# Kernel tuning notes

Hardware: AMD Instinct MI355X
Metric: run time of the kernel (lower is better)

The kernel has to match this reference:

```python
import jax, jax.numpy as jnp
import numpy as np

N = 16384      # total nodes
SEQ = 512      # nodes per graph
NG = 32        # graphs (N = NG*SEQ)
D = 128        # dim_h
H = 8          # heads
E = 262144     # edges
BN_EPS = 1e-5


def _bn(x, g, b):
    # BatchNorm1d, training-mode stats over the node axis (biased var, as torch)
    mu = x.mean(axis=0)
    var = x.var(axis=0)
    return (x - mu) * jax.lax.rsqrt(var + BN_EPS) * g + b


def setup_inputs() -> dict:
    key = jax.random.key(0)
    ks = jax.random.split(key, 24)
    w = lambda k, shp: (jax.random.normal(k, shp, jnp.float32) * 0.05)
    x = jax.random.normal(ks[0], (N, D), jnp.float32)
    # within-graph edges: dst in same graph as src
    src = jax.random.randint(ks[1], (E,), 0, N, dtype=jnp.int32)
    dst = (src // SEQ) * SEQ + jax.random.randint(ks[2], (E,), 0, SEQ, dtype=jnp.int32)
    edge_index = jnp.stack([src, dst])
    edge_attr = jax.random.normal(ks[3], (E, D), jnp.float32)
    return {
        'x': x, 'edge_index': edge_index, 'edge_attr': edge_attr,
        'gin_w1': w(ks[4], (D, D)), 'gin_b1': jnp.zeros((D,), jnp.float32),
        'gin_w2': w(ks[5], (D, D)), 'gin_b2': jnp.zeros((D,), jnp.float32),
        'bn1l_g': jnp.ones((D,), jnp.float32), 'bn1l_b': jnp.zeros((D,), jnp.float32),
        'in_proj_w': w(ks[6], (3 * D, D)), 'in_proj_b': jnp.zeros((3 * D,), jnp.float32),
        'out_proj_w': w(ks[7], (D, D)), 'out_proj_b': jnp.zeros((D,), jnp.float32),
        'bn1a_g': jnp.ones((D,), jnp.float32), 'bn1a_b': jnp.zeros((D,), jnp.float32),
        'ff_w1': w(ks[8], (D, 2 * D)), 'ff_b1': jnp.zeros((2 * D,), jnp.float32),
        'ff_w2': w(ks[9], (2 * D, D)), 'ff_b2': jnp.zeros((D,), jnp.float32),
        'bn2_g': jnp.ones((D,), jnp.float32), 'bn2_b': jnp.zeros((D,), jnp.float32),
    }


def reference(x, edge_index, edge_attr, gin_w1, gin_b1, gin_w2, gin_b2,
              bn1l_g, bn1l_b, in_proj_w, in_proj_b, out_proj_w, out_proj_b,
              bn1a_g, bn1a_b, ff_w1, ff_b1, ff_w2, ff_b2, bn2_g, bn2_b):
    h_in1 = x
    src, dst = edge_index[0], edge_index[1]
    # --- local GINE: aggr_i = sum_{j->i} relu(x_j + e_ji); nn((1+eps)*x + aggr), eps=0
    msg = jax.nn.relu(x[src] + edge_attr)                 # [E, D]
    aggr = jax.ops.segment_sum(msg, dst, num_segments=N)  # [N, D]
    z = x + aggr
    h_local = jax.nn.relu(z @ gin_w1 + gin_b1) @ gin_w2 + gin_b2
    h_local = h_in1 + h_local                # residual (dropout=0)
    h_local = _bn(h_local, bn1l_g, bn1l_b)
    # --- global Transformer attention over dense batch (equal-size graphs => reshape)
    hd = x.reshape(NG, SEQ, D)
    qkv = hd @ in_proj_w.T + in_proj_b       # [NG, SEQ, 3D]
    q, k, v = jnp.split(qkv, 3, axis=-1)
    dh = D // H
    q = q.reshape(NG, SEQ, H, dh)
    k = k.reshape(NG, SEQ, H, dh)
    v = v.reshape(NG, SEQ, H, dh)
    scores = jnp.einsum('bqhd,bkhd->bhqk', q, k) / jnp.sqrt(jnp.float32(dh))
    attn = jax.nn.softmax(scores, axis=-1)
    o = jnp.einsum('bhqk,bkhd->bqhd', attn, v).reshape(NG, SEQ, D)
    h_attn = (o @ out_proj_w.T + out_proj_b).reshape(N, D)
    h_attn = h_in1 + h_attn                  # residual (attn_dropout=0)
    h_attn = _bn(h_attn, bn1a_g, bn1a_b)
    # --- combine + FFN block
    h = h_local + h_attn
    ff = jax.nn.relu(h @ ff_w1 + ff_b1) @ ff_w2 + ff_b2
    h = h + ff
    h = _bn(h, bn2_g, bn2_b)
    return h
```

## Files before the change

kernel.cpp:

```cpp
#include <hip/hip_runtime.h>


#define N_NODES 16384
#define SEQL    512
#define NGRAPH  32
#define DIM     128
#define NHEAD   8
#define DHEAD   16
#define NEDGE   262144
#define BUCKET  64

typedef __bf16 bf16;
typedef __bf16 bf16x8 __attribute__((ext_vector_type(8)));
typedef __bf16 bf16x4 __attribute__((ext_vector_type(4)));
typedef __bf16 bf16x2 __attribute__((ext_vector_type(2)));
typedef float  f32x4  __attribute__((ext_vector_type(4)));

__device__ inline f32x4 mfma16(bf16x8 a, bf16x8 b, f32x4 c) {
  return __builtin_amdgcn_mfma_f32_16x16x32_bf16(a, b, c, 0, 0, 0);
}

__device__ inline void stage_w(const bf16* __restrict__ src0, int stride, int tid,
                               bf16 (*Wlds)[136]) {
  int n = tid >> 1, ch = (tid & 1) * 64;
  const bf16* src = src0 + (size_t)n * stride + ch;
  bf16* dst = &Wlds[n][ch];
#pragma unroll
  for (int j = 0; j < 8; ++j)
    *(bf16x8*)(dst + j * 8) = *(const bf16x8*)(src + j * 8);
}

__global__ __launch_bounds__(256) void prep_k(
    const float* __restrict__ gw1, const float* __restrict__ gw2,
    const float* __restrict__ ipw, const float* __restrict__ opw,
    const float* __restrict__ fw1, const float* __restrict__ fw2,
    bf16* __restrict__ W, int* __restrict__ cnt, float* __restrict__ stats)
{
  int i = blockIdx.x * 256 + threadIdx.x;
  if (i < 16384) {
    W[(i & 127) * 128 + (i >> 7)] = (bf16)gw1[i];
  } else if (i < 32768) {
    int j = i - 16384;
    W[16384 + (j & 127) * 128 + (j >> 7)] = (bf16)gw2[j];
  } else if (i < 81920) {
    W[i] = (bf16)ipw[i - 32768];
  } else if (i < 98304) {
    W[i] = (bf16)opw[i - 81920];
  } else if (i < 131072) {
    int j = i - 98304;
    W[98304 + (j & 255) * 128 + (j >> 8)] = (bf16)fw1[j];
  } else if (i < 163840) {
    int j = i - 131072;
    W[131072 + (j & 127) * 256 + (j >> 7)] = (bf16)fw2[j];
  } else if (i < 163840 + 16384) {
    cnt[i - 163840] = 0;
  } else if (i < 163840 + 16384 + 768) {
    stats[i - 163840 - 16384] = 0.f;
  }
}

__global__ __launch_bounds__(256) void scatter_k(const int* __restrict__ ei,
                                                 int* __restrict__ cnt,
                                                 int2* __restrict__ se)
{
  int e = blockIdx.x * 256 + threadIdx.x;
  if (e < NEDGE) {
    int s = ei[e];
    int d = ei[NEDGE + e];
    int p = atomicAdd(&cnt[d], 1);
    if (p < BUCKET) se[(d << 6) + p] = make_int2(s, e);
  }
}

__global__ __launch_bounds__(256) void aggr_k(
    const float* __restrict__ x, const float* __restrict__ ea,
    const int* __restrict__ cnt, const int2* __restrict__ se,
    bf16* __restrict__ z)
{
  int node = blockIdx.x * 4 + (threadIdx.x >> 6);
  int lane = threadIdx.x & 63;
  int c = lane * 2;
  int n = cnt[node];
  if (n > BUCKET) n = BUCKET;
  int o0 = node << 6, o1 = o0 + n;
  float a0 = 0.f, a1 = 0.f;
  int j = o0;
  for (; j + 4 <= o1; j += 4) {
    int2 p0 = se[j], p1 = se[j + 1], p2 = se[j + 2], p3 = se[j + 3];
    float2 x0 = *(const float2*)(x + (size_t)p0.x * 128 + c);
    float2 e0 = *(const float2*)(ea + (size_t)p0.y * 128 + c);
    float2 x1 = *(const float2*)(x + (size_t)p1.x * 128 + c);
    float2 e1 = *(const float2*)(ea + (size_t)p1.y * 128 + c);
    float2 x2 = *(const float2*)(x + (size_t)p2.x * 128 + c);
    float2 e2 = *(const float2*)(ea + (size_t)p2.y * 128 + c);
    float2 x3 = *(const float2*)(x + (size_t)p3.x * 128 + c);
    float2 e3 = *(const float2*)(ea + (size_t)p3.y * 128 + c);
    a0 += fmaxf(x0.x + e0.x, 0.f) + fmaxf(x1.x + e1.x, 0.f) +
          fmaxf(x2.x + e2.x, 0.f) + fmaxf(x3.x + e3.x, 0.f);
    a1 += fmaxf(x0.y + e0.y, 0.f) + fmaxf(x1.y + e1.y, 0.f) +
          fmaxf(x2.y + e2.y, 0.f) + fmaxf(x3.y + e3.y, 0.f);
  }
  for (; j < o1; ++j) {
    int2 p = se[j];
    float2 xe = *(const float2*)(x + (size_t)p.x * 128 + c);
    float2 ae = *(const float2*)(ea + (size_t)p.y * 128 + c);
    a0 += fmaxf(xe.x + ae.x, 0.f);
    a1 += fmaxf(xe.y + ae.y, 0.f);
  }
  float2 xn = *(const float2*)(x + (size_t)node * 128 + c);
  *(bf16x2*)(z + (size_t)node * 128 + c) =
      (bf16x2){(bf16)(xn.x + a0), (bf16)(xn.y + a1)};
}

__global__ __launch_bounds__(256) void proj_k(
    const bf16* __restrict__ z, const float* __restrict__ x,
    const bf16* __restrict__ W,
    const float* __restrict__ gb1, const float* __restrict__ gb2,
    const float* __restrict__ ipb,
    float* __restrict__ hl, bf16* __restrict__ qb, bf16* __restrict__ kb,
    bf16* __restrict__ vb, float* __restrict__ stats)
{
  __shared__ bf16 Alds[32][136];
  __shared__ bf16 Wlds[128][136];
  __shared__ bf16 Tlds[32][136];
  __shared__ float slds[256];
  int tid = threadIdx.x;
  int wave = tid >> 6, lane = tid & 63, quad = lane >> 4, l16 = lane & 15;
  int rg = wave >> 1, chalf = wave & 1;
  int bid = blockIdx.x;

  if (bid < 512) {
    int m0 = bid * 32;
    slds[tid] = 0.f;
    {
      int r = tid >> 3, c16 = (tid & 7) * 16;
      const bf16* src = z + (size_t)(m0 + r) * 128 + c16;
      *(bf16x8*)&Alds[r][c16]     = *(const bf16x8*)src;
      *(bf16x8*)&Alds[r][c16 + 8] = *(const bf16x8*)(src + 8);
    }
    stage_w(W, 128, tid, Wlds);
    __syncthreads();
    f32x4 acc[4];
#pragma unroll
    for (int t = 0; t < 4; ++t) acc[t] = (f32x4){0.f, 0.f, 0.f, 0.f};
#pragma unroll
    for (int kt = 0; kt < 4; ++kt) {
      bf16x8 af = *(const bf16x8*)&Alds[rg * 16 + l16][kt * 32 + quad * 8];
#pragma unroll
      for (int nt = 0; nt < 4; ++nt) {
        bf16x8 bfr = *(const bf16x8*)&Wlds[chalf * 64 + nt * 16 + l16][kt * 32 + quad * 8];
        acc[nt] = mfma16(af, bfr, acc[nt]);
      }
    }
    __syncthreads();
    int rowl = rg * 16 + quad * 4;
#pragma unroll
    for (int nt = 0; nt < 4; ++nt) {
      int n = chalf * 64 + nt * 16 + l16;
      float bv = gb1[n];
#pragma unroll
      for (int r = 0; r < 4; ++r)
        Tlds[rowl + r][n] = (bf16)fmaxf(acc[nt][r] + bv, 0.f);
    }
    stage_w(W + 16384, 128, tid, Wlds);
    __syncthreads();
#pragma unroll
    for (int t = 0; t < 4; ++t) acc[t] = (f32x4){0.f, 0.f, 0.f, 0.f};
#pragma unroll
    for (int kt = 0; kt < 4; ++kt) {
      bf16x8 af = *(const bf16x8*)&Tlds[rg * 16 + l16][kt * 32 + quad * 8];
#pragma unroll
      for (int nt = 0; nt < 4; ++nt) {
        bf16x8 bfr = *(const bf16x8*)&Wlds[chalf * 64 + nt * 16 + l16][kt * 32 + quad * 8];
        acc[nt] = mfma16(af, bfr, acc[nt]);
      }
    }
    int rowb = m0 + rowl;
#pragma unroll
    for (int nt = 0; nt < 4; ++nt) {
      int n = chalf * 64 + nt * 16 + l16;
      float bv = gb2[n];
      float vals[4];
#pragma unroll
      for (int r = 0; r < 4; ++r) {
        float v = acc[nt][r] + bv + x[(size_t)(rowb + r) * 128 + n];
        vals[r] = v;
        hl[(size_t)(rowb + r) * 128 + n] = v;
      }
      float s = vals[0] + vals[1] + vals[2] + vals[3];
      float q2 = vals[0] * vals[0] + vals[1] * vals[1] +
                 vals[2] * vals[2] + vals[3] * vals[3];
      s += __shfl_xor(s, 16);  s += __shfl_xor(s, 32);
      q2 += __shfl_xor(q2, 16); q2 += __shfl_xor(q2, 32);
      if (quad == 0) {
        atomicAdd(&slds[n * 2], s);
        atomicAdd(&slds[n * 2 + 1], q2);
      }
    }
    __syncthreads();
    if (tid < 128) {
      atomicAdd(&stats[tid], slds[tid * 2]);
      atomicAdd(&stats[128 + tid], slds[tid * 2 + 1]);
    }
  } else {
    int m0 = (bid - 512) * 32;
    {
      int r = tid >> 3, c16 = (tid & 7) * 16;
      const float* src = x + (size_t)(m0 + r) * 128 + c16;
      float4 v0 = *(const float4*)(src);
      float4 v1 = *(const float4*)(src + 4);
      float4 v2 = *(const float4*)(src + 8);
      float4 v3 = *(const float4*)(src + 12);
      *(bf16x8*)&Alds[r][c16] =
          (bf16x8){(bf16)v0.x, (bf16)v0.y, (bf16)v0.z, (bf16)v0.w,
                   (bf16)v1.x, (bf16)v1.y, (bf16)v1.z, (bf16)v1.w};
      *(bf16x8*)&Alds[r][c16 + 8] =
          (bf16x8){(bf16)v2.x, (bf16)v2.y, (bf16)v2.z, (bf16)v2.w,
                   (bf16)v3.x, (bf16)v3.y, (bf16)v3.z, (bf16)v3.w};
    }
    for (int nc = 0; nc < 3; ++nc) {
      if (nc) __syncthreads();
      stage_w(W + 32768 + nc * 16384, 128, tid, Wlds);
      __syncthreads();
      f32x4 acc[4];
#pragma unroll
      for (int t = 0; t < 4; ++t) acc[t] = (f32x4){0.f, 0.f, 0.f, 0.f};
#pragma unroll
      for (int kt = 0; kt < 4; ++kt) {
        bf16x8 af = *(const bf16x8*)&Alds[rg * 16 + l16][kt * 32 + quad * 8];
#pragma unroll
        for (int nt = 0; nt < 4; ++nt) {
          bf16x8 bfr = *(const bf16x8*)&Wlds[chalf * 64 + nt * 16 + l16][kt * 32 + quad * 8];
          acc[nt] = mfma16(af, bfr, acc[nt]);
        }
      }
      bf16* obuf = (nc == 0) ? qb : ((nc == 1) ? kb : vb);
      int rowb = m0 + rg * 16 + quad * 4;
#pragma unroll
      for (int nt = 0; nt < 4; ++nt) {
        int n = chalf * 64 + nt * 16 + l16;
        float bv = ipb[nc * 128 + n];
#pragma unroll
        for (int r = 0; r < 4; ++r)
          obuf[(size_t)(rowb + r) * 128 + n] = (bf16)(acc[nt][r] + bv);
      }
    }
  }
}

template <int NCH, int KCH, bool RELU, int RESID, bool STATS, int OUTMODE>
__global__ __launch_bounds__(256) void gemm_k(
    const float* __restrict__ Aptr, const bf16* __restrict__ Wt,
    const float* __restrict__ bias, const float* __restrict__ resid,
    float* __restrict__ outF, bf16* __restrict__ oq, bf16* __restrict__ okk,
    bf16* __restrict__ ov, float* __restrict__ stats)
{
  constexpr int KIN = KCH * 128;
  constexpr int NLD = NCH * 128;
  __shared__ bf16 Alds[32][136];
  __shared__ bf16 Wlds[128][136];
  __shared__ float slds[256];
  int tid = threadIdx.x;
  int wave = tid >> 6, lane = tid & 63, quad = lane >> 4, l16 = lane & 15;
  int rg = wave >> 1, chalf = wave & 1;
  int m0 = blockIdx.x * 32;
  if (STATS) slds[tid] = 0.f;

  for (int nc = 0; nc < NCH; ++nc) {
    f32x4 acc[4];
#pragma unroll
    for (int t = 0; t < 4; ++t) acc[t] = (f32x4){0.f, 0.f, 0.f, 0.f};
    for (int kc = 0; kc < KCH; ++kc) {
      if (!(nc == 0 && kc == 0)) __syncthreads();
      if (nc == 0 || KCH > 1) {
        int r = tid >> 3, c16 = (tid & 7) * 16;
        const float* src = Aptr + (size_t)(m0 + r) * KIN + kc * 128 + c16;
        float4 v0 = *(const float4*)(src);
        float4 v1 = *(const float4*)(src + 4);
        float4 v2 = *(const float4*)(src + 8);
        float4 v3 = *(const float4*)(src + 12);
        *(bf16x8*)&Alds[r][c16] =
            (bf16x8){(bf16)v0.x, (bf16)v0.y, (bf16)v0.z, (bf16)v0.w,
                     (bf16)v1.x, (bf16)v1.y, (bf16)v1.z, (bf16)v1.w};
        *(bf16x8*)&Alds[r][c16 + 8] =
            (bf16x8){(bf16)v2.x, (bf16)v2.y, (bf16)v2.z, (bf16)v2.w,
                     (bf16)v3.x, (bf16)v3.y, (bf16)v3.z, (bf16)v3.w};
      }
      stage_w(Wt + (size_t)(nc * 128) * KIN + kc * 128, KIN, tid, Wlds);
      __syncthreads();
#pragma unroll
      for (int kt = 0; kt < 4; ++kt) {
        bf16x8 af = *(const bf16x8*)&Alds[rg * 16 + l16][kt * 32 + quad * 8];
#pragma unroll
        for (int nt = 0; nt < 4; ++nt) {
          bf16x8 bfr =
              *(const bf16x8*)&Wlds[chalf * 64 + nt * 16 + l16][kt * 32 + quad * 8];
          acc[nt] = mfma16(af, bfr, acc[nt]);
        }
      }
    }
    int rowb = m0 + rg * 16 + quad * 4;
#pragma unroll
    for (int nt = 0; nt < 4; ++nt) {
      int n = chalf * 64 + nt * 16 + l16;
      int gcol = nc * 128 + n;
      float bv = bias[gcol];
      float vals[4];
#pragma unroll
      for (int r = 0; r < 4; ++r) {
        float v = acc[nt][r] + bv;
        if (RELU) v = fmaxf(v, 0.f);
        if (RESID) v += resid[(size_t)(rowb + r) * 128 + n];
        vals[r] = v;
        if (OUTMODE == 0) {
          outF[(size_t)(rowb + r) * NLD + gcol] = v;
        } else {
          bf16* ob = (nc == 0) ? oq : ((nc == 1) ? okk : ov);
          ob[(size_t)(rowb + r) * 128 + n] = (bf16)v;
        }
      }
      if (STATS) {
        float s = vals[0] + vals[1] + vals[2] + vals[3];
        float q2 = vals[0] * vals[0] + vals[1] * vals[1] +
                   vals[2] * vals[2] + vals[3] * vals[3];
        s += __shfl_xor(s, 16);  s += __shfl_xor(s, 32);
        q2 += __shfl_xor(q2, 16); q2 += __shfl_xor(q2, 32);
        if (quad == 0) {
          atomicAdd(&slds[n * 2], s);
          atomicAdd(&slds[n * 2 + 1], q2);
        }
      }
    }
  }
  if (STATS) {
    __syncthreads();
    if (tid < 128) {
      atomicAdd(&stats[tid], slds[tid * 2]);
      atomicAdd(&stats[128 + tid], slds[tid * 2 + 1]);
    }
  }
}

__global__ __launch_bounds__(256) void attn_k(
    const bf16* __restrict__ qg, const bf16* __restrict__ kg,
    const bf16* __restrict__ vg, float* __restrict__ og)
{
  __shared__ bf16 Klds[512][24];
  __shared__ bf16 Vlds[16][520];
  __shared__ bf16 Plds[4][16][136];
  int b = blockIdx.x;
  int half = b & 1, hh = (b >> 1) & 7, g = b >> 4;
  int tid = threadIdx.x;
  const size_t gbase = (size_t)g * 512 * 128 + hh * 16;
  for (int r = tid; r < 512; r += 256) {
    const bf16* src = kg + gbase + (size_t)r * 128;
    *(bf16x8*)&Klds[r][0] = *(const bf16x8*)src;
    *(bf16x8*)&Klds[r][8] = *(const bf16x8*)(src + 8);
  }
  for (int r = tid; r < 512; r += 256) {
    const bf16* src = vg + gbase + (size_t)r * 128;
    bf16x8 v0 = *(const bf16x8*)src;
    bf16x8 v1 = *(const bf16x8*)(src + 8);
#pragma unroll
    for (int d = 0; d < 8; ++d) { Vlds[d][r] = v0[d]; Vlds[d + 8][r] = v1[d]; }
  }
  __syncthreads();
  int wave = tid >> 6, lane = tid & 63, quad = lane >> 4, l16 = lane & 15;
  const bf16x8 z8 = {};
  for (int it = 0; it < 4; ++it) {
    int qt = half * 16 + it * 4 + wave;
    bf16x8 qf = z8;
    if (quad < 2)
      qf = *(const bf16x8*)(qg + gbase + (size_t)(qt * 16 + l16) * 128 + quad * 8);
    f32x4 S[32];
#pragma unroll
    for (int jt = 0; jt < 32; ++jt) {
      bf16x8 kf = z8;
      if (quad < 2) kf = *(const bf16x8*)&Klds[jt * 16 + l16][quad * 8];
      S[jt] = mfma16(kf, qf, (f32x4){0.f, 0.f, 0.f, 0.f});
    }
    float s0 = 0.f, s1 = 0.f, s2 = 0.f, s3 = 0.f;
#pragma unroll
    for (int jt = 0; jt < 32; ++jt) {
      float e0 = __expf(S[jt][0] * 0.25f);
      float e1 = __expf(S[jt][1] * 0.25f);
      float e2 = __expf(S[jt][2] * 0.25f);
      float e3 = __expf(S[jt][3] * 0.25f);
      S[jt][0] = e0; S[jt][1] = e1; S[jt][2] = e2; S[jt][3] = e3;
      s0 += e0; s1 += e1; s2 += e2; s3 += e3;
    }
    float sm = (s0 + s1) + (s2 + s3);
    sm += __shfl_xor(sm, 16);
    sm += __shfl_xor(sm, 32);
    float rinv = 1.f / sm;
    f32x4 O = (f32x4){0.f, 0.f, 0.f, 0.f};
#pragma unroll
    for (int qd = 0; qd < 4; ++qd) {
#pragma unroll
      for (int jt2 = 0; jt2 < 8; ++jt2) {
        f32x4 sv = S[qd * 8 + jt2];
        bf16x4 pk = {(bf16)sv[0], (bf16)sv[1], (bf16)sv[2], (bf16)sv[3]};
        *(bf16x4*)&Plds[wave][l16][jt2 * 16 + quad * 4] = pk;
      }
#pragma unroll
      for (int kt = 0; kt < 4; ++kt) {
        bf16x8 pf = *(const bf16x8*)&Plds[wave][l16][kt * 32 + quad * 8];
        bf16x8 vf = *(const bf16x8*)&Vlds[l16][qd * 128 + kt * 32 + quad * 8];
        O = mfma16(vf, pf, O);
      }
    }
    *(float4*)(og + (size_t)(g * 512 + qt * 16 + l16) * 128 + hh * 16 + quad * 4) =
        make_float4(O[0] * rinv, O[1] * rinv, O[2] * rinv, O[3] * rinv);
  }
}

__global__ __launch_bounds__(256) void ffn_k(
    const float* __restrict__ hl, const float* __restrict__ ha,
    const bf16* __restrict__ W1, const bf16* __restrict__ W2,
    const float* __restrict__ fb1, const float* __restrict__ fb2,
    const float* __restrict__ stats,
    const float* __restrict__ g1v, const float* __restrict__ b1v,
    const float* __restrict__ g2v, const float* __restrict__ b2v,
    float* __restrict__ h2o, float* __restrict__ so)
{
  __shared__ float Hlds[32][132];
  __shared__ bf16 Ablds[32][136];
  __shared__ bf16 Wlds[128][136];
  __shared__ bf16 Tlds[32][264];
  __shared__ float sc1[128], sh1[128], sc2[128], sh2[128];
  __shared__ float slds[256];
  int tid = threadIdx.x;
  int wave = tid >> 6, lane = tid & 63, quad = lane >> 4, l16 = lane & 15;
  int rg = wave >> 1, chalf = wave & 1;
  int m0 = blockIdx.x * 32;
  slds[tid] = 0.f;
  if (tid < 128) {
    const float inv = 1.f / 16384.f;
    float mu = stats[tid] * inv;
    float var = stats[128 + tid] * inv - mu * mu;
    float s = g1v[tid] * rsqrtf(var + 1e-5f);
    sc1[tid] = s; sh1[tid] = b1v[tid] - mu * s;
    mu = stats[256 + tid] * inv;
    var = stats[384 + tid] * inv - mu * mu;
    s = g2v[tid] * rsqrtf(var + 1e-5f);
    sc2[tid] = s; sh2[tid] = b2v[tid] - mu * s;
  }
  __syncthreads();
  {
    int r = tid >> 3, c0 = (tid & 7) * 16;
    const float* pl = hl + (size_t)(m0 + r) * 128 + c0;
    const float* pa = ha + (size_t)(m0 + r) * 128 + c0;
#pragma unroll
    for (int j = 0; j < 16; j += 8) {
      float4 a0 = *(const float4*)(pl + j);
      float4 a1 = *(const float4*)(pl + j + 4);
      float4 c0v = *(const float4*)(pa + j);
      float4 c1v = *(const float4*)(pa + j + 4);
      int c = c0 + j;
      float h0 = a0.x * sc1[c]     + sh1[c]     + c0v.x * sc2[c]     + sh2[c];
      float h1 = a0.y * sc1[c + 1] + sh1[c + 1] + c0v.y * sc2[c + 1] + sh2[c + 1];
      float h2 = a0.z * sc1[c + 2] + sh1[c + 2] + c0v.z * sc2[c + 2] + sh2[c + 2];
      float h3 = a0.w * sc1[c + 3] + sh1[c + 3] + c0v.w * sc2[c + 3] + sh2[c + 3];
      float h4 = a1.x * sc1[c + 4] + sh1[c + 4] + c1v.x * sc2[c + 4] + sh2[c + 4];
      float h5 = a1.y * sc1[c + 5] + sh1[c + 5] + c1v.y * sc2[c + 5] + sh2[c + 5];
      float h6 = a1.z * sc1[c + 6] + sh1[c + 6] + c1v.z * sc2[c + 6] + sh2[c + 6];
      float h7 = a1.w * sc1[c + 7] + sh1[c + 7] + c1v.w * sc2[c + 7] + sh2[c + 7];
      *(float4*)&Hlds[r][c]     = make_float4(h0, h1, h2, h3);
      *(float4*)&Hlds[r][c + 4] = make_float4(h4, h5, h6, h7);
      *(bf16x8*)&Ablds[r][c] = (bf16x8){(bf16)h0, (bf16)h1, (bf16)h2, (bf16)h3,
                                        (bf16)h4, (bf16)h5, (bf16)h6, (bf16)h7};
    }
  }
  stage_w(W1, 128, tid, Wlds);
  __syncthreads();
  int rowl = rg * 16 + quad * 4;
  f32x4 acc[4];
#pragma unroll
  for (int t = 0; t < 4; ++t) acc[t] = (f32x4){0.f, 0.f, 0.f, 0.f};
#pragma unroll
  for (int kt = 0; kt < 4; ++kt) {
    bf16x8 af = *(const bf16x8*)&Ablds[rg * 16 + l16][kt * 32 + quad * 8];
#pragma unroll
    for (int nt = 0; nt < 4; ++nt) {
      bf16x8 bfr = *(const bf16x8*)&Wlds[chalf * 64 + nt * 16 + l16][kt * 32 + quad * 8];
      acc[nt] = mfma16(af, bfr, acc[nt]);
    }
  }
  __syncthreads();
#pragma unroll
  for (int nt = 0; nt < 4; ++nt) {
    int n = chalf * 64 + nt * 16 + l16;
    float bv = fb1[n];
#pragma unroll
    for (int r = 0; r < 4; ++r)
      Tlds[rowl + r][n] = (bf16)fmaxf(acc[nt][r] + bv, 0.f);
  }
  stage_w(W1 + 128 * 128, 128, tid, Wlds);
  __syncthreads();
#pragma unroll
  for (int t = 0; t < 4; ++t) acc[t] = (f32x4){0.f, 0.f, 0.f, 0.f};
#pragma unroll
  for (int kt = 0; kt < 4; ++kt) {
    bf16x8 af = *(const bf16x8*)&Ablds[rg * 16 + l16][kt * 32 + quad * 8];
#pragma unroll
    for (int nt = 0; nt < 4; ++nt) {
      bf16x8 bfr = *(const bf16x8*)&Wlds[chalf * 64 + nt * 16 + l16][kt * 32 + quad * 8];
      acc[nt] = mfma16(af, bfr, acc[nt]);
    }
  }
  __syncthreads();
#pragma unroll
  for (int nt = 0; nt < 4; ++nt) {
    int n = chalf * 64 + nt * 16 + l16;
    float bv = fb1[128 + n];
#pragma unroll
    for (int r = 0; r < 4; ++r)
      Tlds[rowl + r][128 + n] = (bf16)fmaxf(acc[nt][r] + bv, 0.f);
  }
  stage_w(W2, 256, tid, Wlds);
  __syncthreads();
#pragma unroll
  for (int t = 0; t < 4; ++t) acc[t] = (f32x4){0.f, 0.f, 0.f, 0.f};
#pragma unroll
  for (int kt = 0; kt < 4; ++kt) {
    bf16x8 af = *(const bf16x8*)&Tlds[rg * 16 + l16][kt * 32 + quad * 8];
#pragma unroll
    for (int nt = 0; nt < 4; ++nt) {
      bf16x8 bfr = *(const bf16x8*)&Wlds[chalf * 64 + nt * 16 + l16][kt * 32 + quad * 8];
      acc[nt] = mfma16(af, bfr, acc[nt]);
    }
  }
  __syncthreads();
  stage_w(W2 + 128, 256, tid, Wlds);
  __syncthreads();
#pragma unroll
  for (int kt = 0; kt < 4; ++kt) {
    bf16x8 af = *(const bf16x8*)&Tlds[rg * 16 + l16][128 + kt * 32 + quad * 8];
#pragma unroll
    for (int nt = 0; nt < 4; ++nt) {
      bf16x8 bfr = *(const bf16x8*)&Wlds[chalf * 64 + nt * 16 + l16][kt * 32 + quad * 8];
      acc[nt] = mfma16(af, bfr, acc[nt]);
    }
  }
  int rowb = m0 + rowl;
#pragma unroll
  for (int nt = 0; nt < 4; ++nt) {
    int n = chalf * 64 + nt * 16 + l16;
    float bv = fb2[n];
    float vals[4];
#pragma unroll
    for (int r = 0; r < 4; ++r) {
      float v = acc[nt][r] + bv + Hlds[rowl + r][n];
      vals[r] = v;
      h2o[(size_t)(rowb + r) * 128 + n] = v;
    }
    float s = vals[0] + vals[1] + vals[2] + vals[3];
    float q2 = vals[0] * vals[0] + vals[1] * vals[1] +
               vals[2] * vals[2] + vals[3] * vals[3];
    s += __shfl_xor(s, 16);  s += __shfl_xor(s, 32);
    q2 += __shfl_xor(q2, 16); q2 += __shfl_xor(q2, 32);
    if (quad == 0) {
      atomicAdd(&slds[n * 2], s);
      atomicAdd(&slds[n * 2 + 1], q2);
    }
  }
  __syncthreads();
  if (tid < 128) {
    atomicAdd(&so[tid], slds[tid * 2]);
    atomicAdd(&so[128 + tid], slds[tid * 2 + 1]);
  }
}

__global__ __launch_bounds__(256) void apply_k(
    const float* __restrict__ h2, const float* __restrict__ stats,
    const float* __restrict__ g, const float* __restrict__ b,
    float* __restrict__ out)
{
  __shared__ float sc[128], sh[128];
  int tid = threadIdx.x;
  if (tid < 128) {
    const float inv = 1.f / 16384.f;
    float mu = stats[512 + tid] * inv;
    float var = stats[640 + tid] * inv - mu * mu;
    float s = g[tid] * rsqrtf(var + 1e-5f);
    sc[tid] = s; sh[tid] = b[tid] - mu * s;
  }
  __syncthreads();
  size_t i = ((size_t)blockIdx.x * 256 + tid) * 4;
  int c = (int)(i & 127);
  float4 a = *(const float4*)(h2 + i);
  float4 o;
  o.x = a.x * sc[c] + sh[c];
  o.y = a.y * sc[c + 1] + sh[c + 1];
  o.z = a.z * sc[c + 2] + sh[c + 2];
  o.w = a.w * sc[c + 3] + sh[c + 3];
  *(float4*)(out + i) = o;
}

extern "C" void kernel_launch(void* const* d_in, const int* in_sizes, int n_in,
                              void* d_out, int out_size, void* d_ws, size_t ws_size,
                              hipStream_t stream)
{
  (void)in_sizes; (void)n_in; (void)out_size; (void)ws_size;
  const float* x      = (const float*)d_in[0];
  const int*   ei     = (const int*)d_in[1];
  const float* ea     = (const float*)d_in[2];
  const float* gw1    = (const float*)d_in[3];
  const float* gb1    = (const float*)d_in[4];
  const float* gw2    = (const float*)d_in[5];
  const float* gb2    = (const float*)d_in[6];
  const float* bn1l_g = (const float*)d_in[7];
  const float* bn1l_b = (const float*)d_in[8];
  const float* ipw    = (const float*)d_in[9];
  const float* ipb    = (const float*)d_in[10];
  const float* opw    = (const float*)d_in[11];
  const float* opb    = (const float*)d_in[12];
  const float* bn1a_g = (const float*)d_in[13];
  const float* bn1a_b = (const float*)d_in[14];
  const float* fw1    = (const float*)d_in[15];
  const float* fb1    = (const float*)d_in[16];
  const float* fw2    = (const float*)d_in[17];
  const float* fb2    = (const float*)d_in[18];
  const float* bn2_g  = (const float*)d_in[19];
  const float* bn2_b  = (const float*)d_in[20];

  char* ws = (char*)d_ws;
  const size_t KB = 1024, MB = 1048576;
  bf16*  W     = (bf16*)(ws + 0);
  float* stats = (float*)(ws + 320 * KB);
  int*   cnt   = (int*)(ws + 384 * KB);
  int2*  se    = (int2*)(ws + 1 * MB);
  bf16*  z     = (bf16*)(ws + 9 * MB);
  float* hl    = (float*)(ws + 13 * MB);
  bf16*  qb    = (bf16*)(ws + 21 * MB);
  bf16*  kb    = (bf16*)(ws + 25 * MB);
  bf16*  vb    = (bf16*)(ws + 29 * MB);
  float* ob    = (float*)(ws + 33 * MB);
  float* ha    = (float*)(ws + 41 * MB);
  float* h2    = ob;
  float* out   = (float*)d_out;

  prep_k<<<708, 256, 0, stream>>>(gw1, gw2, ipw, opw, fw1, fw2, W, cnt, stats);
  scatter_k<<<1024, 256, 0, stream>>>(ei, cnt, se);
  aggr_k<<<4096, 256, 0, stream>>>(x, ea, cnt, se, z);
  proj_k<<<1024, 256, 0, stream>>>(z, x, W, gb1, gb2, ipb,
                                   hl, qb, kb, vb, stats + 0);
  attn_k<<<512, 256, 0, stream>>>(qb, kb, vb, ob);
  gemm_k<1, 1, false, 1, true, 0><<<512, 256, 0, stream>>>(
      ob, W + 81920, opb, x, ha, nullptr, nullptr, nullptr, stats + 256);
  ffn_k<<<512, 256, 0, stream>>>(hl, ha, W + 98304, W + 131072, fb1, fb2,
                                 stats, bn1l_g, bn1l_b, bn1a_g, bn1a_b,
                                 h2, stats + 512);
  apply_k<<<2048, 256, 0, stream>>>(h2, stats, bn2_g, bn2_b, out);
}
```

Baseline: 380.1 us.

## Load weight MFMA fragments straight from global into registers, drop LDS staging

Weight tiles are no longer copied cooperatively into a shared-memory buffer. Instead, each wave loads the B-operand fragments it needs directly from global memory into registers (64 VGPRs of bf16x8). This removes the weight LDS buffer and several __syncthreads barriers in proj_k, the output-projection kernel and ffn_k, and the templated gemm_k is replaced by a specialised op_k. In exchange, each weight element is fetched by the two waves that share a column half rather than once per block, and register pressure rises, which may lower occupancy.

New measurement: 390.4 us. +2.7%, slower.

```diff
diff --git a/kernel.cpp b/kernel.cpp
--- a/kernel.cpp
+++ b/kernel.cpp
@@ -20,14 +20,16 @@
   return __builtin_amdgcn_mfma_f32_16x16x32_bf16(a, b, c, 0, 0, 0);
 }
 
-__device__ inline void stage_w(const bf16* __restrict__ src0, int stride, int tid,
-                               bf16 (*Wlds)[136]) {
-  int n = tid >> 1, ch = (tid & 1) * 64;
-  const bf16* src = src0 + (size_t)n * stride + ch;
-  bf16* dst = &Wlds[n][ch];
-#pragma unroll
-  for (int j = 0; j < 8; ++j)
-    *(bf16x8*)(dst + j * 8) = *(const bf16x8*)(src + j * 8);
+__device__ inline void load_wfrags(const bf16* __restrict__ Wt, int stride,
+                                   int chalf, int l16, int quad,
+                                   bf16x8 wf[4][4]) {
+#pragma unroll
+  for (int nt = 0; nt < 4; ++nt) {
+    const bf16* rp = Wt + (size_t)(chalf * 64 + nt * 16 + l16) * stride + quad * 8;
+#pragma unroll
+    for (int kt = 0; kt < 4; ++kt)
+      wf[nt][kt] = *(const bf16x8*)(rp + kt * 32);
+  }
 }
 
 __global__ __launch_bounds__(256) void prep_k(
@@ -121,13 +123,14 @@
     bf16* __restrict__ vb, float* __restrict__ stats)
 {
   __shared__ bf16 Alds[32][136];
-  __shared__ bf16 Wlds[128][136];
   __shared__ bf16 Tlds[32][136];
   __shared__ float slds[256];
   int tid = threadIdx.x;
   int wave = tid >> 6, lane = tid & 63, quad = lane >> 4, l16 = lane & 15;
   int rg = wave >> 1, chalf = wave & 1;
   int bid = blockIdx.x;
+  bf16x8 wf[4][4];
+  f32x4 acc[4];
 
   if (bid < 512) {
     int m0 = bid * 32;
@@ -138,21 +141,17 @@
       *(bf16x8*)&Alds[r][c16]     = *(const bf16x8*)src;
       *(bf16x8*)&Alds[r][c16 + 8] = *(const bf16x8*)(src + 8);
     }
-    stage_w(W, 128, tid, Wlds);
+    load_wfrags(W, 128, chalf, l16, quad, wf);
     __syncthreads();
-    f32x4 acc[4];
 #pragma unroll
     for (int t = 0; t < 4; ++t) acc[t] = (f32x4){0.f, 0.f, 0.f, 0.f};
 #pragma unroll
     for (int kt = 0; kt < 4; ++kt) {
       bf16x8 af = *(const bf16x8*)&Alds[rg * 16 + l16][kt * 32 + quad * 8];
 #pragma unroll
-      for (int nt = 0; nt < 4; ++nt) {
-        bf16x8 bfr = *(const bf16x8*)&Wlds[chalf * 64 + nt * 16 + l16][kt * 32 + quad * 8];
-        acc[nt] = mfma16(af, bfr, acc[nt]);
-      }
-    }
-    __syncthreads();
+      for (int nt = 0; nt < 4; ++nt)
+        acc[nt] = mfma16(af, wf[nt][kt], acc[nt]);
+    }
     int rowl = rg * 16 + quad * 4;
 #pragma unroll
     for (int nt = 0; nt < 4; ++nt) {
@@ -162,7 +161,7 @@
       for (int r = 0; r < 4; ++r)
         Tlds[rowl + r][n] = (bf16)fmaxf(acc[nt][r] + bv, 0.f);
     }
-    stage_w(W + 16384, 128, tid, Wlds);
+    load_wfrags(W + 16384, 128, chalf, l16, quad, wf);
     __syncthreads();
 #pragma unroll
     for (int t = 0; t < 4; ++t) acc[t] = (f32x4){0.f, 0.f, 0.f, 0.f};
@@ -170,10 +169,8 @@
     for (int kt = 0; kt < 4; ++kt) {
       bf16x8 af = *(const bf16x8*)&Tlds[rg * 16 + l16][kt * 32 + quad * 8];
 #pragma unroll
-      for (int nt = 0; nt < 4; ++nt) {
-        bf16x8 bfr = *(const bf16x8*)&Wlds[chalf * 64 + nt * 16 + l16][kt * 32 + quad * 8];
-        acc[nt] = mfma16(af, bfr, acc[nt]);
-      }
+      for (int nt = 0; nt < 4; ++nt)
+        acc[nt] = mfma16(af, wf[nt][kt], acc[nt]);
     }
     int rowb = m0 + rowl;
 #pragma unroll
@@ -218,24 +215,21 @@
           (bf16x8){(bf16)v2.x, (bf16)v2.y, (bf16)v2.z, (bf16)v2.w,
                    (bf16)v3.x, (bf16)v3.y, (bf16)v3.z, (bf16)v3.w};
     }
+    __syncthreads();
+    int rowb = m0 + rg * 16 + quad * 4;
+#pragma unroll
     for (int nc = 0; nc < 3; ++nc) {
-      if (nc) __syncthreads();
-      stage_w(W + 32768 + nc * 16384, 128, tid, Wlds);
-      __syncthreads();
-      f32x4 acc[4];
+      load_wfrags(W + 32768 + nc * 16384, 128, chalf, l16, quad, wf);
 #pragma unroll
       for (int t = 0; t < 4; ++t) acc[t] = (f32x4){0.f, 0.f, 0.f, 0.f};
 #pragma unroll
       for (int kt = 0; kt < 4; ++kt) {
         bf16x8 af = *(const bf16x8*)&Alds[rg * 16 + l16][kt * 32 + quad * 8];
 #pragma unroll
-        for (int nt = 0; nt < 4; ++nt) {
-          bf16x8 bfr = *(const bf16x8*)&Wlds[chalf * 64 + nt * 16 + l16][kt * 32 + quad * 8];
-          acc[nt] = mfma16(af, bfr, acc[nt]);
-        }
+        for (int nt = 0; nt < 4; ++nt)
+          acc[nt] = mfma16(af, wf[nt][kt], acc[nt]);
       }
       bf16* obuf = (nc == 0) ? qb : ((nc == 1) ? kb : vb);
-      int rowb = m0 + rg * 16 + quad * 4;
 #pragma unroll
       for (int nt = 0; nt < 4; ++nt) {
         int n = chalf * 64 + nt * 16 + l16;
@@ -248,96 +242,71 @@
   }
 }
 
-template <int NCH, int KCH, bool RELU, int RESID, bool STATS, int OUTMODE>
-__global__ __launch_bounds__(256) void gemm_k(
+__global__ __launch_bounds__(256) void op_k(
     const float* __restrict__ Aptr, const bf16* __restrict__ Wt,
     const float* __restrict__ bias, const float* __restrict__ resid,
-    float* __restrict__ outF, bf16* __restrict__ oq, bf16* __restrict__ okk,
-    bf16* __restrict__ ov, float* __restrict__ stats)
-{
-  constexpr int KIN = KCH * 128;
-  constexpr int NLD = NCH * 128;
+    float* __restrict__ outF, float* __restrict__ stats)
+{
   __shared__ bf16 Alds[32][136];
-  __shared__ bf16 Wlds[128][136];
   __shared__ float slds[256];
   int tid = threadIdx.x;
   int wave = tid >> 6, lane = tid & 63, quad = lane >> 4, l16 = lane & 15;
   int rg = wave >> 1, chalf = wave & 1;
   int m0 = blockIdx.x * 32;
-  if (STATS) slds[tid] = 0.f;
-
-  for (int nc = 0; nc < NCH; ++nc) {
-    f32x4 acc[4];
-#pragma unroll
-    for (int t = 0; t < 4; ++t) acc[t] = (f32x4){0.f, 0.f, 0.f, 0.f};
-    for (int kc = 0; kc < KCH; ++kc) {
-      if (!(nc == 0 && kc == 0)) __syncthreads();
-      if (nc == 0 || KCH > 1) {
-        int r = tid >> 3, c16 = (tid & 7) * 16;
-        const float* src = Aptr + (size_t)(m0 + r) * KIN + kc * 128 + c16;
-        float4 v0 = *(const float4*)(src);
-        float4 v1 = *(const float4*)(src + 4);
-        float4 v2 = *(const float4*)(src + 8);
-        float4 v3 = *(const float4*)(src + 12);
-        *(bf16x8*)&Alds[r][c16] =
-            (bf16x8){(bf16)v0.x, (bf16)v0.y, (bf16)v0.z, (bf16)v0.w,
-                     (bf16)v1.x, (bf16)v1.y, (bf16)v1.z, (bf16)v1.w};
-        *(bf16x8*)&Alds[r][c16 + 8] =
-            (bf16x8){(bf16)v2.x, (bf16)v2.y, (bf16)v2.z, (bf16)v2.w,
-                     (bf16)v3.x, (bf16)v3.y, (bf16)v3.z, (bf16)v3.w};
-      }
-      stage_w(Wt + (size_t)(nc * 128) * KIN + kc * 128, KIN, tid, Wlds);
-      __syncthreads();
-#pragma unroll
-      for (int kt = 0; kt < 4; ++kt) {
-        bf16x8 af = *(const bf16x8*)&Alds[rg * 16 + l16][kt * 32 + quad * 8];
-#pragma unroll
-        for (int nt = 0; nt < 4; ++nt) {
-          bf16x8 bfr =
-              *(const bf16x8*)&Wlds[chalf * 64 + nt * 16 + l16][kt * 32 + quad * 8];
-          acc[nt] = mfma16(af, bfr, acc[nt]);
-        }
-      }
-    }
-    int rowb = m0 + rg * 16 + quad * 4;
-#pragma unroll
-    for (int nt = 0; nt < 4; ++nt) {
-      int n = chalf * 64 + nt * 16 + l16;
-      int gcol = nc * 128 + n;
-      float bv = bias[gcol];
-      float vals[4];
-#pragma unroll
-      for (int r = 0; r < 4; ++r) {
-        float v = acc[nt][r] + bv;
-        if (RELU) v = fmaxf(v, 0.f);
-        if (RESID) v += resid[(size_t)(rowb + r) * 128 + n];
-        vals[r] = v;
-        if (OUTMODE == 0) {
-          outF[(size_t)(rowb + r) * NLD + gcol] = v;
-        } else {
-          bf16* ob = (nc == 0) ? oq : ((nc == 1) ? okk : ov);
-          ob[(size_t)(rowb + r) * 128 + n] = (bf16)v;
-        }
-      }
-      if (STATS) {
-        float s = vals[0] + vals[1] + vals[2] + vals[3];
-        float q2 = vals[0] * vals[0] + vals[1] * vals[1] +
-                   vals[2] * vals[2] + vals[3] * vals[3];
-        s += __shfl_xor(s, 16);  s += __shfl_xor(s, 32);
-        q2 += __shfl_xor(q2, 16); q2 += __shfl_xor(q2, 32);
-        if (quad == 0) {
-          atomicAdd(&slds[n * 2], s);
-          atomicAdd(&slds[n * 2 + 1], q2);
-        }
-      }
-    }
-  }
-  if (STATS) {
-    __syncthreads();
-    if (tid < 128) {
-      atomicAdd(&stats[tid], slds[tid * 2]);
-      atomicAdd(&stats[128 + tid], slds[tid * 2 + 1]);
-    }
+  slds[tid] = 0.f;
+  {
+    int r = tid >> 3, c16 = (tid & 7) * 16;
+    const float* src = Aptr + (size_t)(m0 + r) * 128 + c16;
+    float4 v0 = *(const float4*)(src);
+    float4 v1 = *(const float4*)(src + 4);
+    float4 v2 = *(const float4*)(src + 8);
+    float4 v3 = *(const float4*)(src + 12);
+    *(bf16x8*)&Alds[r][c16] =
+        (bf16x8){(bf16)v0.x, (bf16)v0.y, (bf16)v0.z, (bf16)v0.w,
+                 (bf16)v1.x, (bf16)v1.y, (bf16)v1.z, (bf16)v1.w};
+    *(bf16x8*)&Alds[r][c16 + 8] =
+        (bf16x8){(bf16)v2.x, (bf16)v2.y, (bf16)v2.z, (bf16)v2.w,
+                 (bf16)v3.x, (bf16)v3.y, (bf16)v3.z, (bf16)v3.w};
+  }
+  bf16x8 wf[4][4];
+  load_wfrags(Wt, 128, chalf, l16, quad, wf);
+  __syncthreads();
+  f32x4 acc[4];
+#pragma unroll
+  for (int t = 0; t < 4; ++t) acc[t] = (f32x4){0.f, 0.f, 0.f, 0.f};
+#pragma unroll
+  for (int kt = 0; kt < 4; ++kt) {
+    bf16x8 af = *(const bf16x8*)&Alds[rg * 16 + l16][kt * 32 + quad * 8];
+#pragma unroll
+    for (int nt = 0; nt < 4; ++nt)
+      acc[nt] = mfma16(af, wf[nt][kt], acc[nt]);
+  }
+  int rowb = m0 + rg * 16 + quad * 4;
+#pragma unroll
+  for (int nt = 0; nt < 4; ++nt) {
+    int n = chalf * 64 + nt * 16 + l16;
+    float bv = bias[n];
+    float vals[4];
+#pragma unroll
+    for (int r = 0; r < 4; ++r) {
+      float v = acc[nt][r] + bv + resid[(size_t)(rowb + r) * 128 + n];
+      vals[r] = v;
+      outF[(size_t)(rowb + r) * 128 + n] = v;
+    }
+    float s = vals[0] + vals[1] + vals[2] + vals[3];
+    float q2 = vals[0] * vals[0] + vals[1] * vals[1] +
+               vals[2] * vals[2] + vals[3] * vals[3];
+    s += __shfl_xor(s, 16);  s += __shfl_xor(s, 32);
+    q2 += __shfl_xor(q2, 16); q2 += __shfl_xor(q2, 32);
+    if (quad == 0) {
+      atomicAdd(&slds[n * 2], s);
+      atomicAdd(&slds[n * 2 + 1], q2);
+    }
+  }
+  __syncthreads();
+  if (tid < 128) {
+    atomicAdd(&stats[tid], slds[tid * 2]);
+    atomicAdd(&stats[128 + tid], slds[tid * 2 + 1]);
   }
 }
 
@@ -425,7 +394,6 @@
 {
   __shared__ float Hlds[32][132];
   __shared__ bf16 Ablds[32][136];
-  __shared__ bf16 Wlds[128][136];
   __shared__ bf16 Tlds[32][264];
   __shared__ float sc1[128], sh1[128], sc2[128], sh2[128];
   __shared__ float slds[256];
@@ -445,6 +413,8 @@
     s = g2v[tid] * rsqrtf(var + 1e-5f);
     sc2[tid] = s; sh2[tid] = b2v[tid] - mu * s;
   }
+  bf16x8 wf[4][4];
+  load_wfrags(W1, 128, chalf, l16, quad, wf);
   __syncthreads();
   {
     int r = tid >> 3, c0 = (tid & 7) * 16;
@@ -471,7 +441,6 @@
                                         (bf16)h4, (bf16)h5, (bf16)h6, (bf16)h7};
     }
   }
-  stage_w(W1, 128, tid, Wlds);
   __syncthreads();
   int rowl = rg * 16 + quad * 4;
   f32x4 acc[4];
@@ -481,12 +450,9 @@
   for (int kt = 0; kt < 4; ++kt) {
     bf16x8 af = *(const bf16x8*)&Ablds[rg * 16 + l16][kt * 32 + quad * 8];
 #pragma unroll
-    for (int nt = 0; nt < 4; ++nt) {
-      bf16x8 bfr = *(const bf16x8*)&Wlds[chalf * 64 + nt * 16 + l16][kt * 32 + quad * 8];
-      acc[nt] = mfma16(af, bfr, acc[nt]);
-    }
-  }
-  __syncthreads();
+    for (int nt = 0; nt < 4; ++nt)
+      acc[nt] = mfma16(af, wf[nt][kt], acc[nt]);
+  }
 #pragma unroll
   for (int nt = 0; nt < 4; ++nt) {
     int n = chalf * 64 + nt * 16 + l16;
@@ -495,20 +461,16 @@
     for (int r = 0; r < 4; ++r)
       Tlds[rowl + r][n] = (bf16)fmaxf(acc[nt][r] + bv, 0.f);
   }
-  stage_w(W1 + 128 * 128, 128, tid, Wlds);
-  __syncthreads();
+  load_wfrags(W1 + 128 * 128, 128, chalf, l16, quad, wf);
 #pragma unroll
   for (int t = 0; t < 4; ++t) acc[t] = (f32x4){0.f, 0.f, 0.f, 0.f};
 #pragma unroll
   for (int kt = 0; kt < 4; ++kt) {
     bf16x8 af = *(const bf16x8*)&Ablds[rg * 16 + l16][kt * 32 + quad * 8];
 #pragma unroll
-    for (int nt = 0; nt < 4; ++nt) {
-      bf16x8 bfr = *(const bf16x8*)&Wlds[chalf * 64 + nt * 16 + l16][kt * 32 + quad * 8];
-      acc[nt] = mfma16(af, bfr, acc[nt]);
-    }
-  }
-  __syncthreads();
+    for (int nt = 0; nt < 4; ++nt)
+      acc[nt] = mfma16(af, wf[nt][kt], acc[nt]);
+  }
 #pragma unroll
   for (int nt = 0; nt < 4; ++nt) {
     int n = chalf * 64 + nt * 16 + l16;
@@ -517,7 +479,7 @@
     for (int r = 0; r < 4; ++r)
       Tlds[rowl + r][128 + n] = (bf16)fmaxf(acc[nt][r] + bv, 0.f);
   }
-  stage_w(W2, 256, tid, Wlds);
+  load_wfrags(W2, 256, chalf, l16, quad, wf);
   __syncthreads();
 #pragma unroll
   for (int t = 0; t < 4; ++t) acc[t] = (f32x4){0.f, 0.f, 0.f, 0.f};
@@ -525,22 +487,16 @@
   for (int kt = 0; kt < 4; ++kt) {
     bf16x8 af = *(const bf16x8*)&Tlds[rg * 16 + l16][kt * 32 + quad * 8];
 #pragma unroll
-    for (int nt = 0; nt < 4; ++nt) {
-      bf16x8 bfr = *(const bf16x8*)&Wlds[chalf * 64 + nt * 16 + l16][kt * 32 + quad * 8];
-      acc[nt] = mfma16(af, bfr, acc[nt]);
-    }
-  }
-  __syncthreads();
-  stage_w(W2 + 128, 256, tid, Wlds);
-  __syncthreads();
+    for (int nt = 0; nt < 4; ++nt)
+      acc[nt] = mfma16(af, wf[nt][kt], acc[nt]);
+  }
+  load_wfrags(W2 + 128, 256, chalf, l16, quad, wf);
 #pragma unroll
   for (int kt = 0; kt < 4; ++kt) {
     bf16x8 af = *(const bf16x8*)&Tlds[rg * 16 + l16][128 + kt * 32 + quad * 8];
 #pragma unroll
-    for (int nt = 0; nt < 4; ++nt) {
-      bf16x8 bfr = *(const bf16x8*)&Wlds[chalf * 64 + nt * 16 + l16][kt * 32 + quad * 8];
-      acc[nt] = mfma16(af, bfr, acc[nt]);
-    }
+    for (int nt = 0; nt < 4; ++nt)
+      acc[nt] = mfma16(af, wf[nt][kt], acc[nt]);
   }
   int rowb = m0 + rowl;
 #pragma unroll
@@ -646,8 +602,7 @@
   proj_k<<<1024, 256, 0, stream>>>(z, x, W, gb1, gb2, ipb,
                                    hl, qb, kb, vb, stats + 0);
   attn_k<<<512, 256, 0, stream>>>(qb, kb, vb, ob);
-  gemm_k<1, 1, false, 1, true, 0><<<512, 256, 0, stream>>>(
-      ob, W + 81920, opb, x, ha, nullptr, nullptr, nullptr, stats + 256);
+  op_k<<<512, 256, 0, stream>>>(ob, W + 81920, opb, x, ha, stats + 256);
   ffn_k<<<512, 256, 0, stream>>>(hl, ha, W + 98304, W + 131072, fb1, fb2,
                                  stats, bn1l_g, bn1l_b, bn1a_g, bn1a_b,
                                  h2, stats + 512);
```
